# Performance work log

Hardware: AMD Instinct MI355X
Metric: run time of the kernel (lower is better)

## Reference

```python
import jax, jax.numpy as jnp
import numpy as np

N = 20000
DEG = 16
E = N * DEG
IN_DIM = 512
OUT_DIM = 512
H = 4
D = OUT_DIM // H            # head_dim = 128
POS_DIM = 3
M_ROPE = D // (POS_DIM * 2) # 21
D_ROPE = POS_DIM * 2 * M_ROPE  # 126 (2 trailing dims unrotated)
ROPE_BASE = 10000.0

INV_FREQ = jnp.exp(-jnp.arange(M_ROPE, dtype=jnp.float32) * (np.log(ROPE_BASE) / M_ROPE))


def _rope(t, pos):
    # t: (N, D, H), pos: (N, POS_DIM)
    n = t.shape[0]
    angles = pos[:, :, None] * INV_FREQ[None, None, :]        # (N, POS_DIM, M)
    cos = jnp.cos(angles)[..., None]                           # (N, POS_DIM, M, 1)
    sin = jnp.sin(angles)[..., None]
    part = t[:, :D_ROPE, :].reshape(n, POS_DIM, M_ROPE, 2, H)
    even, odd = part[..., 0, :], part[..., 1, :]
    rot_even = even * cos - odd * sin
    rot_odd = even * sin + odd * cos
    rot = jnp.stack((rot_even, rot_odd), axis=3).reshape(n, D_ROPE, H)
    return jnp.concatenate([rot, t[:, D_ROPE:, :]], axis=1)


def setup_inputs() -> dict:
    key = jax.random.key(0)
    ks = jax.random.split(key, 12)
    x = jax.random.normal(ks[0], (N, IN_DIM), jnp.float32)
    pos = jax.random.uniform(ks[1], (N, POS_DIM), jnp.float32) * 100.0
    rows = jnp.repeat(jnp.arange(N, dtype=jnp.int32), DEG)  # sorted, every node has DEG out-edges
    cols = jax.random.randint(ks[2], (E,), 0, N, dtype=jnp.int32)
    s = 1.0 / np.sqrt(IN_DIM)
    Wq = jax.random.normal(ks[3], (OUT_DIM, IN_DIM), jnp.float32) * s
    Wk = jax.random.normal(ks[4], (OUT_DIM, IN_DIM), jnp.float32) * s
    Wv = jax.random.normal(ks[5], (OUT_DIM, IN_DIM), jnp.float32) * s
    Wo = jax.random.normal(ks[6], (OUT_DIM, OUT_DIM), jnp.float32) * s
    bq = jax.random.normal(ks[7], (OUT_DIM,), jnp.float32) * 0.01
    bk = jax.random.normal(ks[8], (OUT_DIM,), jnp.float32) * 0.01
    bv = jax.random.normal(ks[9], (OUT_DIM,), jnp.float32) * 0.01
    bo = jax.random.normal(ks[10], (OUT_DIM,), jnp.float32) * 0.01
    return {"x": x, "pos": pos, "rows": rows, "cols": cols,
            "Wq": Wq, "bq": bq, "Wk": Wk, "bk": bk, "Wv": Wv, "bv": bv, "Wo": Wo, "bo": bo}


def reference(x, pos, rows, cols, Wq, bq, Wk, bk, Wv, bv, Wo, bo):
    n = x.shape[0]
    q = (x @ Wq.T + bq).reshape(n, D, H)
    k = (x @ Wk.T + bk).reshape(n, D, H)
    v = (x @ Wv.T + bv).reshape(n, D, H)
    # scaling by sqrt(k.size(1)) == sqrt(head_dim)
    q = q / jnp.sqrt(jnp.asarray(D, q.dtype))
    q = _rope(q, pos)
    k = _rope(k, pos)
    # per-edge scores: s[e,h] = sum_d q[rows[e],d,h] * k[cols[e],d,h]
    scores = jnp.einsum('edh,edh->eh', q[rows], k[cols])  # (E, H)
    # row-wise sparse softmax per head
    row_max = jax.ops.segment_max(scores, rows, num_segments=n, indices_are_sorted=True)
    p = jnp.exp(scores - row_max[rows])
    denom = jax.ops.segment_sum(p, rows, num_segments=n, indices_are_sorted=True)
    attn = p / denom[rows]                                 # (E, H)
    # bspmm: y[i,d,h] = sum_{e: rows[e]=i} attn[e,h] * v[cols[e],d,h]
    y = jax.ops.segment_sum(attn[:, None, :] * v[cols], rows, num_segments=n, indices_are_sorted=True)
    out = y.reshape(n, OUT_DIM) @ Wo.T + bo
    return out
```

## Files before the change

kernel.cpp:

```cpp
#include <hip/hip_runtime.h>
#include <hip/hip_bf16.h>

#define NN 20000
#define DEG 16
#define KD 512
#define OD 512
#define NH 4
#define DH 128
#define DROPE 126

#define BM 128
#define BN 128
#define BK 64

typedef unsigned short u16;
typedef unsigned int u32;
typedef __attribute__((ext_vector_type(8))) short short8;
typedef __attribute__((ext_vector_type(4))) float f32x4;

__device__ __forceinline__ float b2f(u16 u){ return __uint_as_float((u32)u << 16); }
__device__ __forceinline__ u16 f2b(float f){
  u32 x = __float_as_uint(f);
  return (u16)((x + 0x7fffu + ((x >> 16) & 1u)) >> 16);
}
__device__ __forceinline__ void up8(uint4 u, float* f){
  f[0]=__uint_as_float(u.x<<16); f[1]=__uint_as_float(u.x&0xffff0000u);
  f[2]=__uint_as_float(u.y<<16); f[3]=__uint_as_float(u.y&0xffff0000u);
  f[4]=__uint_as_float(u.z<<16); f[5]=__uint_as_float(u.z&0xffff0000u);
  f[6]=__uint_as_float(u.w<<16); f[7]=__uint_as_float(u.w&0xffff0000u);
}
__device__ __forceinline__ uint4 cvt8(const float* s){
  uint4 a = *(const uint4*)s;
  uint4 b = *(const uint4*)(s + 4);
  uint4 o;
  o.x = (u32)f2b(__uint_as_float(a.x)) | ((u32)f2b(__uint_as_float(a.y)) << 16);
  o.y = (u32)f2b(__uint_as_float(a.z)) | ((u32)f2b(__uint_as_float(a.w)) << 16);
  o.z = (u32)f2b(__uint_as_float(b.x)) | ((u32)f2b(__uint_as_float(b.y)) << 16);
  o.w = (u32)f2b(__uint_as_float(b.z)) | ((u32)f2b(__uint_as_float(b.w)) << 16);
  return o;
}

__device__ __forceinline__ void load_lds16(const u16* g, u16* l) {
  __builtin_amdgcn_global_load_lds(
      (const __attribute__((address_space(1))) void*)g,
      (__attribute__((address_space(3))) void*)l, 16, 0, 0);
}

struct ConvJob {
  const float* x;  u16* xb;
  const float* w[4]; u16* wb[4];
  const float* b[4]; u16* bb[4];
};
__global__ __launch_bounds__(256) void conv_all(ConvJob j) {
  const int b = blockIdx.x;
  if (b < 5000) {
    const int i8 = (b * 256 + threadIdx.x) * 8;
    *(uint4*)(j.xb + i8) = cvt8(j.x + i8);
  } else if (b < 5512) {
    const int t = b - 5000;
    const int wsel = t >> 7;
    const int i8 = ((t & 127) * 256 + threadIdx.x) * 8;
    if (wsel < 3) {
      *(uint4*)(j.wb[wsel] + i8) = cvt8(j.w[wsel] + i8);
    } else {
      const int o = i8 >> 9, cp = i8 & 511;
      const int h = cp >> 7, d0 = cp & 127;
      const float* src = j.w[3] + (size_t)o * 512 + h;
      float tmp[8];
      #pragma unroll
      for (int t2 = 0; t2 < 8; t2++) tmp[t2] = src[(size_t)(d0 + t2) * 4];
      uint4 ov;
      ov.x = (u32)f2b(tmp[0]) | ((u32)f2b(tmp[1]) << 16);
      ov.y = (u32)f2b(tmp[2]) | ((u32)f2b(tmp[3]) << 16);
      ov.z = (u32)f2b(tmp[4]) | ((u32)f2b(tmp[5]) << 16);
      ov.w = (u32)f2b(tmp[6]) | ((u32)f2b(tmp[7]) << 16);
      *(uint4*)(j.wb[3] + i8) = ov;
    }
  } else {
    const int vsel = threadIdx.x >> 6;
    const int i8 = (threadIdx.x & 63) * 8;
    *(uint4*)(j.bb[vsel] + i8) = cvt8(j.b[vsel] + i8);
  }
}

__global__ __launch_bounds__(256, 2) void gemm_k(
    const u16* __restrict__ A,
    const u16* __restrict__ W0, const u16* __restrict__ B0,
    const u16* __restrict__ W1, const u16* __restrict__ B1,
    const u16* __restrict__ W2, const u16* __restrict__ B2,
    const float* __restrict__ pos,
    u16* __restrict__ o0, u16* __restrict__ o1, u16* __restrict__ o2,
    int M)
{
  __shared__ __align__(16) char smem[65536];
  __shared__ float posS[BM*3];
  __shared__ float freqS[21];

  const int b = blockIdx.x;
  const int xcd = b & 7, rem = b >> 3;
  const int rowT = (rem / 12)*8 + xcd;
  const int sub = rem % 12;
  const int colT = sub & 3, w = sub >> 2;
  if (rowT*BM >= M) return;

  const int tid = threadIdx.x;
  const int wave = tid >> 6, lane = tid & 63;
  const int wr = wave >> 1, wc = wave & 1;
  const int lm = lane & 15, lq = lane >> 4;
  const u16* W  = (w == 0) ? W0 : ((w == 1) ? W1 : W2);
  const u16* Bi = (w == 0) ? B0 : ((w == 1) ? B1 : B2);
  const int emode = w;
  u16* outQKV = (w == 0) ? o0 : ((w == 1) ? o1 : o2);

  f32x4 acc[4][4];
  #pragma unroll
  for (int i = 0; i < 4; i++)
    #pragma unroll
    for (int jj = 0; jj < 4; jj++)
      acc[i][jj] = (f32x4){0.f, 0.f, 0.f, 0.f};

  if (emode < 2) {
    if (tid < BM) {
      int gr = rowT*BM + tid; if (gr >= M) gr = M - 1;
      posS[tid*3+0] = pos[gr*3+0];
      posS[tid*3+1] = pos[gr*3+1];
      posS[tid*3+2] = pos[gr*3+2];
    }
    if (tid >= BM && tid < BM + 21)
      freqS[tid - BM] = __expf(-(float)(tid - BM) * 0.43858763676077064f);
  }
  __builtin_amdgcn_sched_barrier(0);
  asm volatile("s_waitcnt vmcnt(0)" ::: "memory");

  auto stage = [&](int bufi, int kt) {
    u16* Asb = (u16*)(smem + bufi*32768);
    u16* Bsb = Asb + BM*BK;
    #pragma unroll
    for (int it = 0; it < 4; it++) {
      const int chunk = it*256 + wave*64 + lane;
      const int row = chunk >> 3, gseg = (chunk & 7) ^ (row & 7);
      int gr = rowT*BM + row; if (gr >= M) gr = M - 1;
      load_lds16(A + (size_t)gr*KD + kt + gseg*8,
                 Asb + (size_t)(it*256 + wave*64)*8);
    }
    #pragma unroll
    for (int it = 0; it < 4; it++) {
      const int chunk = it*256 + wave*64 + lane;
      const int row = chunk >> 3, gseg = (chunk & 7) ^ (row & 7);
      load_lds16(W + (size_t)(colT*BN + row)*KD + kt + gseg*8,
                 Bsb + (size_t)(it*256 + wave*64)*8);
    }
  };

  stage(0, 0);

  for (int t = 0; t < 8; t++) {
    const int cur = t & 1;
    if (t < 7) stage(cur ^ 1, (t + 1) * BK);
    __builtin_amdgcn_sched_barrier(0);
    if (t < 7) asm volatile("s_waitcnt vmcnt(8)" ::: "memory");
    else       asm volatile("s_waitcnt vmcnt(0)" ::: "memory");
    __builtin_amdgcn_s_barrier();
    __builtin_amdgcn_sched_barrier(0);

    const u16* Asb = (const u16*)(smem + cur*32768);
    const u16* Bsb = Asb + BM*BK;
    #pragma unroll
    for (int kk = 0; kk < BK; kk += 32) {
      const int ks = kk >> 3;
      short8 af[4], bfr[4];
      #pragma unroll
      for (int i = 0; i < 4; i++) {
        const int ra = wr*64 + i*16 + lm;
        af[i] = *(const short8*)(Asb + (size_t)(ra*8 + ((ks + lq) ^ (ra & 7)))*8);
      }
      #pragma unroll
      for (int i = 0; i < 4; i++) {
        const int rb = wc*64 + i*16 + lm;
        bfr[i] = *(const short8*)(Bsb + (size_t)(rb*8 + ((ks + lq) ^ (rb & 7)))*8);
      }
      #pragma unroll
      for (int mi = 0; mi < 4; mi++)
        #pragma unroll
        for (int ni = 0; ni < 4; ni++)
          acc[mi][ni] = __builtin_amdgcn_mfma_f32_16x16x32_bf16(af[mi], bfr[ni], acc[mi][ni], 0, 0, 0);
    }
    __builtin_amdgcn_sched_barrier(0);
    __builtin_amdgcn_s_barrier();
  }

  float bvv[4];
  #pragma unroll
  for (int ni = 0; ni < 4; ni++)
    bvv[ni] = b2f(Bi[colT*BN + wc*64 + ni*16 + lm]);

  u16* Cs = (u16*)smem;

  #pragma unroll
  for (int mi = 0; mi < 4; mi++) {
    #pragma unroll
    for (int ni = 0; ni < 4; ni++) {
      const int cloc = wc*64 + ni*16 + lm;
      const int h = cloc & 3, dloc = cloc >> 2;
      const int d = colT*32 + dloc;
      #pragma unroll
      for (int r = 0; r < 4; r++) {
        const int rloc = wr*64 + mi*16 + lq*4 + r;
        float v = acc[mi][ni][r] + bvv[ni];
        if (emode == 0) v *= 0.08838834764831845f;
        float vr = v;
        if (emode < 2) {
          const float partner = __shfl_xor(v, 4);
          if (d < DROPE) {
            const int pp = d / 42, rem2 = d - pp*42, m = rem2 >> 1, par = rem2 & 1;
            const float ang = posS[rloc*3 + pp] * freqS[m];
            float sn, cs; __sincosf(ang, &sn, &cs);
            vr = par ? (v*cs + partner*sn) : (v*cs - partner*sn);
          }
        }
        Cs[rloc*144 + h*36 + dloc] = f2b(vr);
      }
    }
  }
  __syncthreads();
  #pragma unroll
  for (int pass = 0; pass < 8; pass++) {
    const int c2 = pass*256 + tid;
    const int dd8 = c2 & 3, h = (c2 >> 2) & 3, rloc = c2 >> 4;
    const int grow = rowT*BM + rloc;
    if (grow < M) {
      uint2 a = *(const uint2*)(Cs + rloc*144 + h*36 + dd8*8);
      uint2 b2 = *(const uint2*)(Cs + rloc*144 + h*36 + dd8*8 + 4);
      *(uint4*)(outQKV + ((size_t)grow*NH + h)*DH + colT*32 + dd8*8)
          = make_uint4(a.x, a.y, b2.x, b2.y);
    }
  }
}

__global__ __launch_bounds__(256, 4) void gemm_o(
    const u16* __restrict__ A, const u16* __restrict__ W,
    const u16* __restrict__ Bi, float* __restrict__ out, int M)
{
  __shared__ __align__(16) u16 As[BM*BK];
  __shared__ __align__(16) u16 Bs[BN*BK];

  const int b = blockIdx.x;
  const int xcd = b & 7, rem = b >> 3;
  const int rowT = (rem >> 2)*8 + xcd, colT = rem & 3;
  if (rowT*BM >= M) return;

  const int tid = threadIdx.x;
  const int wave = tid >> 6, lane = tid & 63;
  const int wr = wave >> 1, wc = wave & 1;
  const int lm = lane & 15, lq = lane >> 4;

  f32x4 acc[4][4];
  #pragma unroll
  for (int i = 0; i < 4; i++)
    #pragma unroll
    for (int jj = 0; jj < 4; jj++)
      acc[i][jj] = (f32x4){0.f, 0.f, 0.f, 0.f};

  for (int kt = 0; kt < KD; kt += BK) {
    #pragma unroll
    for (int it = 0; it < 4; it++) {
      const int chunk = it*256 + wave*64 + lane;
      const int row = chunk >> 3, gseg = (chunk & 7) ^ (row & 7);
      int gr = rowT*BM + row; if (gr >= M) gr = M - 1;
      load_lds16(A + (size_t)gr*KD + kt + gseg*8,
                 As + (size_t)(it*256 + wave*64)*8);
    }
    #pragma unroll
    for (int it = 0; it < 4; it++) {
      const int chunk = it*256 + wave*64 + lane;
      const int row = chunk >> 3, gseg = (chunk & 7) ^ (row & 7);
      load_lds16(W + (size_t)(colT*BN + row)*KD + kt + gseg*8,
                 Bs + (size_t)(it*256 + wave*64)*8);
    }
    __syncthreads();
    #pragma unroll
    for (int kk = 0; kk < BK; kk += 32) {
      const int ks = kk >> 3;
      short8 af[4], bfr[4];
      #pragma unroll
      for (int i = 0; i < 4; i++) {
        const int ra = wr*64 + i*16 + lm;
        af[i] = *(const short8*)(As + (size_t)(ra*8 + ((ks + lq) ^ (ra & 7)))*8);
      }
      #pragma unroll
      for (int i = 0; i < 4; i++) {
        const int rb = wc*64 + i*16 + lm;
        bfr[i] = *(const short8*)(Bs + (size_t)(rb*8 + ((ks + lq) ^ (rb & 7)))*8);
      }
      #pragma unroll
      for (int mi = 0; mi < 4; mi++)
        #pragma unroll
        for (int ni = 0; ni < 4; ni++)
          acc[mi][ni] = __builtin_amdgcn_mfma_f32_16x16x32_bf16(af[mi], bfr[ni], acc[mi][ni], 0, 0, 0);
    }
    __syncthreads();
  }

  float bvv[4];
  #pragma unroll
  for (int ni = 0; ni < 4; ni++)
    bvv[ni] = b2f(Bi[colT*BN + wc*64 + ni*16 + lm]);

  #pragma unroll
  for (int mi = 0; mi < 4; mi++)
    #pragma unroll
    for (int ni = 0; ni < 4; ni++) {
      const int Cg = colT*BN + wc*64 + ni*16 + lm;
      #pragma unroll
      for (int r = 0; r < 4; r++) {
        const int grow = rowT*BM + wr*64 + mi*16 + lq*4 + r;
        if (grow < M) out[(size_t)grow*OD + Cg] = acc[mi][ni][r] + bvv[ni];
      }
    }
}


__global__ __launch_bounds__(256, 3) void edge_score(
    const int* __restrict__ cols, const u16* __restrict__ qf,
    const u16* __restrict__ kf, float* __restrict__ aw)
{
  const int b = blockIdx.x;
  const int xcd = b & 7;
  const int head = xcd >> 1;
  const int nbase = (b >> 3) * 32 + (xcd & 1) * 16;
  const int wave = threadIdx.x >> 6, lane = threadIdx.x & 63;
  const int g = lane >> 4, l16 = lane & 15;
  const int n = nbase + wave*4 + g;

  const int col = cols[n*DEG + l16];
  const uint4 qv = *(const uint4*)(qf + ((size_t)n*NH + head)*DH + l16*8);

  uint4 kreg[16];
  #pragma unroll
  for (int jj = 0; jj < 16; jj++) {
    const int cj = __shfl(col, g*16 + jj);
    kreg[jj] = *(const uint4*)(kf + ((size_t)cj*NH + head)*DH + l16*8);
  }
  float qa[8]; up8(qv, qa);

  float s = 0.f;
  #pragma unroll
  for (int jj = 0; jj < 16; jj++) {
    float ka[8]; up8(kreg[jj], ka);
    float pr = qa[0]*ka[0] + qa[1]*ka[1] + qa[2]*ka[2] + qa[3]*ka[3]
             + qa[4]*ka[4] + qa[5]*ka[5] + qa[6]*ka[6] + qa[7]*ka[7];
    pr += __shfl_xor(pr, 1);
    pr += __shfl_xor(pr, 2);
    pr += __shfl_xor(pr, 4);
    pr += __shfl_xor(pr, 8);
    s = (l16 == jj) ? pr : s;
  }

  float mx = s;
  #pragma unroll
  for (int msk = 1; msk < 16; msk <<= 1) mx = fmaxf(mx, __shfl_xor(mx, msk));
  float p = expf(s - mx);
  float dn = p;
  #pragma unroll
  for (int msk = 1; msk < 16; msk <<= 1) dn += __shfl_xor(dn, msk);
  aw[(size_t)(n*NH + head)*DEG + l16] = p / dn;
}

__global__ __launch_bounds__(256, 3) void edge_gather(
    const int* __restrict__ cols, const u16* __restrict__ vf,
    const float* __restrict__ aw, u16* __restrict__ y)
{
  const int b = blockIdx.x;
  const int xcd = b & 7;
  const int head = xcd >> 1;
  const int nbase = (b >> 3) * 32 + (xcd & 1) * 16;
  const int wave = threadIdx.x >> 6, lane = threadIdx.x & 63;
  const int g = lane >> 4, l16 = lane & 15;
  const int n = nbase + wave*4 + g;

  const int col = cols[n*DEG + l16];
  const float a_l = aw[(size_t)(n*NH + head)*DEG + l16];

  uint4 vreg[16];
  #pragma unroll
  for (int jj = 0; jj < 16; jj++) {
    const int cj = __shfl(col, g*16 + jj);
    vreg[jj] = *(const uint4*)(vf + ((size_t)cj*NH + head)*DH + l16*8);
  }

  float ya[8];
  #pragma unroll
  for (int t = 0; t < 8; t++) ya[t] = 0.f;
  #pragma unroll
  for (int jj = 0; jj < 16; jj++) {
    const float a = __shfl(a_l, g*16 + jj);
    float va[8]; up8(vreg[jj], va);
    #pragma unroll
    for (int t = 0; t < 8; t++) ya[t] += a*va[t];
  }
  u32 pk[4];
  #pragma unroll
  for (int t = 0; t < 4; t++)
    pk[t] = (u32)f2b(ya[2*t]) | ((u32)f2b(ya[2*t+1]) << 16);
  *(uint4*)(y + ((size_t)n*NH + head)*DH + l16*8) = make_uint4(pk[0], pk[1], pk[2], pk[3]);
}

extern "C" void kernel_launch(void* const* d_in, const int* in_sizes, int n_in,
                              void* d_out, int out_size, void* d_ws, size_t ws_size,
                              hipStream_t stream) {
  (void)in_sizes; (void)n_in; (void)out_size; (void)ws_size;
  const float* x   = (const float*)d_in[0];
  const float* pos = (const float*)d_in[1];
  const int* cols = (const int*)d_in[3];
  const float* Wq = (const float*)d_in[4];
  const float* bq = (const float*)d_in[5];
  const float* Wk = (const float*)d_in[6];
  const float* bk = (const float*)d_in[7];
  const float* Wv = (const float*)d_in[8];
  const float* bv = (const float*)d_in[9];
  const float* Wo = (const float*)d_in[10];
  const float* bo = (const float*)d_in[11];

  char* ws = (char*)d_ws;
  size_t off = 0;
  auto carve = [&](size_t bytes) { char* p = ws + off; off += (bytes + 15) & ~(size_t)15; return p; };
  u16* xb   = (u16*)carve((size_t)NN*KD*2);
  u16* Wqb  = (u16*)carve((size_t)OD*KD*2);
  u16* Wkb  = (u16*)carve((size_t)OD*KD*2);
  u16* Wvb  = (u16*)carve((size_t)OD*KD*2);
  u16* Wob  = (u16*)carve((size_t)OD*OD*2);
  u16* bqb  = (u16*)carve((size_t)OD*2);
  u16* bkb  = (u16*)carve((size_t)OD*2);
  u16* bvb  = (u16*)carve((size_t)OD*2);
  u16* bob  = (u16*)carve((size_t)OD*2);
  u16* qf   = (u16*)carve((size_t)NN*OD*2);
  u16* kf   = (u16*)carve((size_t)NN*OD*2);
  u16* vf   = (u16*)carve((size_t)NN*OD*2);
  u16* y    = (u16*)carve((size_t)NN*OD*2);
  float* aw = (float*)carve((size_t)NN*NH*DEG*4);

  ConvJob cj;
  cj.x = x; cj.xb = xb;
  cj.w[0]=Wq; cj.w[1]=Wk; cj.w[2]=Wv; cj.w[3]=Wo;
  cj.wb[0]=Wqb; cj.wb[1]=Wkb; cj.wb[2]=Wvb; cj.wb[3]=Wob;
  cj.b[0]=bq; cj.b[1]=bk; cj.b[2]=bv; cj.b[3]=bo;
  cj.bb[0]=bqb; cj.bb[1]=bkb; cj.bb[2]=bvb; cj.bb[3]=bob;
  conv_all<<<dim3(5513), 256, 0, stream>>>(cj);

  gemm_k<<<dim3(1920), 256, 0, stream>>>(xb, Wqb, bqb, Wkb, bkb, Wvb, bvb, pos,
                                         qf, kf, vf, NN);
  edge_score<<<dim3(5000), 256, 0, stream>>>(cols, qf, kf, aw);
  edge_gather<<<dim3(5000), 256, 0, stream>>>(cols, vf, aw, y);
  gemm_o<<<dim3(640), 256, 0, stream>>>(y, Wob, bob, (float*)d_out, NN);
}
```

Measured before the change: 237.5 us.

## Fuse Q/K/V projections per block to reuse the staged activation tile

Each block of the QKV GEMM now computes all three projections for its row/column tile, loading the x tile into shared memory once and streaming three weight tiles alongside it, with three accumulator sets. This cuts global reads of the activation tile by three and reduces the grid to 640 blocks. In exchange it drops the double-buffered prefetch pipeline in favour of a single-buffered loop with plain syncthreads, triples accumulator register pressure (192 floats) under a 2-blocks-per-SM launch bound, and serialises three epilogue passes through the shared staging buffer.

```diff
diff --git a/kernel.cpp b/kernel.cpp
--- a/kernel.cpp
+++ b/kernel.cpp
@@ -98,141 +98,134 @@
 
   const int b = blockIdx.x;
   const int xcd = b & 7, rem = b >> 3;
-  const int rowT = (rem / 12)*8 + xcd;
-  const int sub = rem % 12;
-  const int colT = sub & 3, w = sub >> 2;
+  const int rowT = (rem >> 2)*8 + xcd;
+  const int colT = rem & 3;
   if (rowT*BM >= M) return;
 
   const int tid = threadIdx.x;
   const int wave = tid >> 6, lane = tid & 63;
   const int wr = wave >> 1, wc = wave & 1;
   const int lm = lane & 15, lq = lane >> 4;
-  const u16* W  = (w == 0) ? W0 : ((w == 1) ? W1 : W2);
-  const u16* Bi = (w == 0) ? B0 : ((w == 1) ? B1 : B2);
-  const int emode = w;
-  u16* outQKV = (w == 0) ? o0 : ((w == 1) ? o1 : o2);
-
-  f32x4 acc[4][4];
-  #pragma unroll
-  for (int i = 0; i < 4; i++)
-    #pragma unroll
-    for (int jj = 0; jj < 4; jj++)
-      acc[i][jj] = (f32x4){0.f, 0.f, 0.f, 0.f};
-
-  if (emode < 2) {
-    if (tid < BM) {
-      int gr = rowT*BM + tid; if (gr >= M) gr = M - 1;
-      posS[tid*3+0] = pos[gr*3+0];
-      posS[tid*3+1] = pos[gr*3+1];
-      posS[tid*3+2] = pos[gr*3+2];
-    }
-    if (tid >= BM && tid < BM + 21)
-      freqS[tid - BM] = __expf(-(float)(tid - BM) * 0.43858763676077064f);
-  }
-  __builtin_amdgcn_sched_barrier(0);
-  asm volatile("s_waitcnt vmcnt(0)" ::: "memory");
-
-  auto stage = [&](int bufi, int kt) {
-    u16* Asb = (u16*)(smem + bufi*32768);
-    u16* Bsb = Asb + BM*BK;
+  const u16* Wp[3] = { W0, W1, W2 };
+
+  f32x4 acc[3][4][4];
+  #pragma unroll
+  for (int w = 0; w < 3; w++)
+    #pragma unroll
+    for (int i = 0; i < 4; i++)
+      #pragma unroll
+      for (int jj = 0; jj < 4; jj++)
+        acc[w][i][jj] = (f32x4){0.f, 0.f, 0.f, 0.f};
+
+  if (tid < BM) {
+    int gr = rowT*BM + tid; if (gr >= M) gr = M - 1;
+    posS[tid*3+0] = pos[gr*3+0];
+    posS[tid*3+1] = pos[gr*3+1];
+    posS[tid*3+2] = pos[gr*3+2];
+  }
+  if (tid >= BM && tid < BM + 21)
+    freqS[tid - BM] = __expf(-(float)(tid - BM) * 0.43858763676077064f);
+
+  u16* As = (u16*)smem;
+
+  for (int kt = 0; kt < KD; kt += BK) {
     #pragma unroll
     for (int it = 0; it < 4; it++) {
-      const int chunk = it*256 + wave*64 + lane;
+      const int chunk = it*256 + tid;
       const int row = chunk >> 3, gseg = (chunk & 7) ^ (row & 7);
       int gr = rowT*BM + row; if (gr >= M) gr = M - 1;
       load_lds16(A + (size_t)gr*KD + kt + gseg*8,
-                 Asb + (size_t)(it*256 + wave*64)*8);
-    }
-    #pragma unroll
-    for (int it = 0; it < 4; it++) {
-      const int chunk = it*256 + wave*64 + lane;
-      const int row = chunk >> 3, gseg = (chunk & 7) ^ (row & 7);
-      load_lds16(W + (size_t)(colT*BN + row)*KD + kt + gseg*8,
-                 Bsb + (size_t)(it*256 + wave*64)*8);
-    }
-  };
-
-  stage(0, 0);
-
-  for (int t = 0; t < 8; t++) {
-    const int cur = t & 1;
-    if (t < 7) stage(cur ^ 1, (t + 1) * BK);
-    __builtin_amdgcn_sched_barrier(0);
-    if (t < 7) asm volatile("s_waitcnt vmcnt(8)" ::: "memory");
-    else       asm volatile("s_waitcnt vmcnt(0)" ::: "memory");
-    __builtin_amdgcn_s_barrier();
-    __builtin_amdgcn_sched_barrier(0);
-
-    const u16* Asb = (const u16*)(smem + cur*32768);
-    const u16* Bsb = Asb + BM*BK;
-    #pragma unroll
-    for (int kk = 0; kk < BK; kk += 32) {
-      const int ks = kk >> 3;
-      short8 af[4], bfr[4];
+                 As + (size_t)(it*256 + wave*64)*8);
+    }
+    #pragma unroll
+    for (int w = 0; w < 3; w++) {
+      u16* Bsw = (u16*)(smem + (1 + w)*16384);
+      #pragma unroll
+      for (int it = 0; it < 4; it++) {
+        const int chunk = it*256 + tid;
+        const int row = chunk >> 3, gseg = (chunk & 7) ^ (row & 7);
+        load_lds16(Wp[w] + (size_t)(colT*BN + row)*KD + kt + gseg*8,
+                   Bsw + (size_t)(it*256 + wave*64)*8);
+      }
+    }
+    __syncthreads();
+    #pragma unroll
+    for (int kk = 0; kk < 2; kk++) {
+      const int ks = kk*4;
+      short8 af[4];
       #pragma unroll
       for (int i = 0; i < 4; i++) {
         const int ra = wr*64 + i*16 + lm;
-        af[i] = *(const short8*)(Asb + (size_t)(ra*8 + ((ks + lq) ^ (ra & 7)))*8);
-      }
-      #pragma unroll
-      for (int i = 0; i < 4; i++) {
-        const int rb = wc*64 + i*16 + lm;
-        bfr[i] = *(const short8*)(Bsb + (size_t)(rb*8 + ((ks + lq) ^ (rb & 7)))*8);
-      }
-      #pragma unroll
-      for (int mi = 0; mi < 4; mi++)
+        af[i] = *(const short8*)(As + (size_t)(ra*8 + ((ks + lq) ^ (ra & 7)))*8);
+      }
+      #pragma unroll
+      for (int w = 0; w < 3; w++) {
+        const u16* Bsw = (const u16*)(smem + (1 + w)*16384);
+        short8 bfr[4];
         #pragma unroll
-        for (int ni = 0; ni < 4; ni++)
-          acc[mi][ni] = __builtin_amdgcn_mfma_f32_16x16x32_bf16(af[mi], bfr[ni], acc[mi][ni], 0, 0, 0);
-    }
-    __builtin_amdgcn_sched_barrier(0);
-    __builtin_amdgcn_s_barrier();
-  }
-
-  float bvv[4];
-  #pragma unroll
-  for (int ni = 0; ni < 4; ni++)
-    bvv[ni] = b2f(Bi[colT*BN + wc*64 + ni*16 + lm]);
-
+        for (int i = 0; i < 4; i++) {
+          const int rb = wc*64 + i*16 + lm;
+          bfr[i] = *(const short8*)(Bsw + (size_t)(rb*8 + ((ks + lq) ^ (rb & 7)))*8);
+        }
+        #pragma unroll
+        for (int mi = 0; mi < 4; mi++)
+          #pragma unroll
+          for (int ni = 0; ni < 4; ni++)
+            acc[w][mi][ni] = __builtin_amdgcn_mfma_f32_16x16x32_bf16(af[mi], bfr[ni], acc[w][mi][ni], 0, 0, 0);
+      }
+    }
+    __syncthreads();
+  }
+
+  const u16* Bb[3] = { B0, B1, B2 };
+  u16* Ob[3] = { o0, o1, o2 };
   u16* Cs = (u16*)smem;
 
   #pragma unroll
-  for (int mi = 0; mi < 4; mi++) {
-    #pragma unroll
-    for (int ni = 0; ni < 4; ni++) {
-      const int cloc = wc*64 + ni*16 + lm;
-      const int h = cloc & 3, dloc = cloc >> 2;
-      const int d = colT*32 + dloc;
-      #pragma unroll
-      for (int r = 0; r < 4; r++) {
-        const int rloc = wr*64 + mi*16 + lq*4 + r;
-        float v = acc[mi][ni][r] + bvv[ni];
-        if (emode == 0) v *= 0.08838834764831845f;
-        float vr = v;
-        if (emode < 2) {
-          const float partner = __shfl_xor(v, 4);
-          if (d < DROPE) {
-            const int pp = d / 42, rem2 = d - pp*42, m = rem2 >> 1, par = rem2 & 1;
-            const float ang = posS[rloc*3 + pp] * freqS[m];
-            float sn, cs; __sincosf(ang, &sn, &cs);
-            vr = par ? (v*cs + partner*sn) : (v*cs - partner*sn);
+  for (int w = 0; w < 3; w++) {
+    if (w) __syncthreads();
+    float bvv[4];
+    #pragma unroll
+    for (int ni = 0; ni < 4; ni++)
+      bvv[ni] = b2f(Bb[w][colT*BN + wc*64 + ni*16 + lm]);
+    #pragma unroll
+    for (int mi = 0; mi < 4; mi++) {
+      #pragma unroll
+      for (int ni = 0; ni < 4; ni++) {
+        const int cloc = wc*64 + ni*16 + lm;
+        const int h = cloc & 3, dloc = cloc >> 2;
+        const int d = colT*32 + dloc;
+        #pragma unroll
+        for (int r = 0; r < 4; r++) {
+          const int rloc = wr*64 + mi*16 + lq*4 + r;
+          float v = acc[w][mi][ni][r] + bvv[ni];
+          if (w == 0) v *= 0.08838834764831845f;
+          float vr = v;
+          if (w < 2) {
+            const float partner = __shfl_xor(v, 4);
+            if (d < DROPE) {
+              const int pp = d / 42, rem2 = d - pp*42, m = rem2 >> 1, par = rem2 & 1;
+              const float ang = posS[rloc*3 + pp] * freqS[m];
+              float sn, cs; __sincosf(ang, &sn, &cs);
+              vr = par ? (v*cs + partner*sn) : (v*cs - partner*sn);
+            }
           }
+          Cs[rloc*144 + h*36 + dloc] = f2b(vr);
         }
-        Cs[rloc*144 + h*36 + dloc] = f2b(vr);
-      }
-    }
-  }
-  __syncthreads();
-  #pragma unroll
-  for (int pass = 0; pass < 8; pass++) {
-    const int c2 = pass*256 + tid;
-    const int dd8 = c2 & 3, h = (c2 >> 2) & 3, rloc = c2 >> 4;
-    const int grow = rowT*BM + rloc;
-    if (grow < M) {
-      uint2 a = *(const uint2*)(Cs + rloc*144 + h*36 + dd8*8);
-      uint2 b2 = *(const uint2*)(Cs + rloc*144 + h*36 + dd8*8 + 4);
-      *(uint4*)(outQKV + ((size_t)grow*NH + h)*DH + colT*32 + dd8*8)
-          = make_uint4(a.x, a.y, b2.x, b2.y);
+      }
+    }
+    __syncthreads();
+    #pragma unroll
+    for (int pass = 0; pass < 8; pass++) {
+      const int c2 = pass*256 + tid;
+      const int dd8 = c2 & 3, h = (c2 >> 2) & 3, rloc = c2 >> 4;
+      const int grow = rowT*BM + rloc;
+      if (grow < M) {
+        uint2 a = *(const uint2*)(Cs + rloc*144 + h*36 + dd8*8);
+        uint2 b2 = *(const uint2*)(Cs + rloc*144 + h*36 + dd8*8 + 4);
+        *(uint4*)(Ob[w] + ((size_t)grow*NH + h)*DH + colT*32 + dd8*8)
+            = make_uint4(a.x, a.y, b2.x, b2.y);
+      }
     }
   }
 }
@@ -264,7 +257,7 @@
   for (int kt = 0; kt < KD; kt += BK) {
     #pragma unroll
     for (int it = 0; it < 4; it++) {
-      const int chunk = it*256 + wave*64 + lane;
+      const int chunk = it*256 + tid;
       const int row = chunk >> 3, gseg = (chunk & 7) ^ (row & 7);
       int gr = rowT*BM + row; if (gr >= M) gr = M - 1;
       load_lds16(A + (size_t)gr*KD + kt + gseg*8,
@@ -272,7 +265,7 @@
     }
     #pragma unroll
     for (int it = 0; it < 4; it++) {
-      const int chunk = it*256 + wave*64 + lane;
+      const int chunk = it*256 + tid;
       const int row = chunk >> 3, gseg = (chunk & 7) ^ (row & 7);
       load_lds16(W + (size_t)(colT*BN + row)*KD + kt + gseg*8,
                  Bs + (size_t)(it*256 + wave*64)*8);
@@ -447,8 +440,8 @@
   cj.bb[0]=bqb; cj.bb[1]=bkb; cj.bb[2]=bvb; cj.bb[3]=bob;
   conv_all<<<dim3(5513), 256, 0, stream>>>(cj);
 
-  gemm_k<<<dim3(1920), 256, 0, stream>>>(xb, Wqb, bqb, Wkb, bkb, Wvb, bvb, pos,
-                                         qf, kf, vf, NN);
+  gemm_k<<<dim3(640), 256, 0, stream>>>(xb, Wqb, bqb, Wkb, bkb, Wvb, bvb, pos,
+                                        qf, kf, vf, NN);
   edge_score<<<dim3(5000), 256, 0, stream>>>(cols, qf, kf, aw);
   edge_gather<<<dim3(5000), 256, 0, stream>>>(cols, vf, aw, y);
   gemm_o<<<dim3(640), 256, 0, stream>>>(y, Wob, bob, (float*)d_out, NN);
```

Result: slower. 247.5 us (+4.2%).
